# Kernel tuning notes

Hardware: AMD Instinct MI355X
Metric: run time of the kernel (lower is better)

## Reference

```python
import jax, jax.numpy as jnp
import numpy as np

B, S, D, P = 4, 2048, 1024, 1024

def setup_inputs() -> dict:
    key = jax.random.key(0)
    k1, k2, k3, k4 = jax.random.split(key, 4)
    x = jax.random.normal(k1, (B, S, D), dtype=jnp.float32)
    # nn.Linear weight is (out, in); store transposed (in, out) for x @ W
    scale = 1.0 / np.sqrt(D)
    Wq = jax.random.normal(k2, (D, P), dtype=jnp.float32) * scale
    Wk = jax.random.normal(k3, (D, P), dtype=jnp.float32) * scale
    Wv = jax.random.normal(k4, (D, P), dtype=jnp.float32) * scale
    return {"x": x, "Wq": Wq, "Wk": Wk, "Wv": Wv}

def reference(x, Wq, Wk, Wv):
    # projections (no bias)
    q = x @ Wq  # (B,S,P)
    k = x @ Wk
    v = x @ Wv
    scores = jnp.einsum('bsd,btd->bst', q, k)  # (B,S,S)
    seq = x.shape[1]
    causal = jnp.triu(jnp.ones((seq, seq), dtype=bool), k=1)
    scores = jnp.where(causal, -jnp.inf, scores)
    scores = scores / jnp.sqrt(jnp.asarray(P, dtype=scores.dtype))
    attn = jax.nn.softmax(scores, axis=-1)
    # dropout_prob=0.0 -> identity
    context = jnp.einsum('bst,btd->bsd', attn, v)  # (B,S,P)
    return context
```

## Files before the change

kernel.cpp:

```cpp
#include <hip/hip_runtime.h>
#include <hip/hip_bf16.h>


#define BDIM 4
#define SDIM 2048
#define DDIM 1024
#define PDIM 1024

typedef __attribute__((ext_vector_type(8))) short bf16x8;
typedef __attribute__((ext_vector_type(4))) float f32x4;
typedef __attribute__((ext_vector_type(16))) float f32x16;

__device__ __forceinline__ unsigned short f2bf(float f) {
    union { float f; unsigned int u; } v; v.f = f;
    unsigned int u = v.u;
    unsigned int r = (u + 0x7fffu + ((u >> 16) & 1u)) >> 16;
    return (unsigned short)r;
}

__device__ __forceinline__ float bf2f(unsigned short h) {
    union { unsigned int u; float f; } v;
    v.u = ((unsigned int)h) << 16;
    return v.f;
}

__device__ __forceinline__ void async16(const unsigned short* g, unsigned short* l) {
    __builtin_amdgcn_global_load_lds(
        (const __attribute__((address_space(1))) unsigned int*)g,
        (__attribute__((address_space(3))) unsigned int*)l,
        16, 0, 0);
}

__global__ __launch_bounds__(256) void prep_kernel(const float* __restrict__ x,
                                                   const float* __restrict__ W0,
                                                   const float* __restrict__ W1,
                                                   const float* __restrict__ W2,
                                                   unsigned short* __restrict__ Xb,
                                                   unsigned short* __restrict__ WT,
                                                   float* __restrict__ Lrow) {
    int bid = blockIdx.x;
    if (bid < 4096) {
        size_t i = (size_t)bid * 256 + threadIdx.x;
        float4 a = ((const float4*)x)[2 * i];
        float4 b = ((const float4*)x)[2 * i + 1];
        bf16x8 o;
        o[0] = (short)f2bf(a.x); o[1] = (short)f2bf(a.y);
        o[2] = (short)f2bf(a.z); o[3] = (short)f2bf(a.w);
        o[4] = (short)f2bf(b.x); o[5] = (short)f2bf(b.y);
        o[6] = (short)f2bf(b.z); o[7] = (short)f2bf(b.w);
        ((bf16x8*)Xb)[i] = o;
    } else if (bid < 4864) {
        int idx = bid - 4096;
        int wz = idx >> 8;
        int t  = idx & 255;
        const float* W = (wz == 0) ? W0 : (wz == 1) ? W1 : W2;
        unsigned short* Tz = WT + (size_t)wz * DDIM * PDIM;
        __shared__ float tle[64 * 65];
        int r0 = (t >> 4) * 64, c0 = (t & 15) * 64;
#pragma unroll
        for (int kk = 0; kk < 4; kk++) {
            int it = (int)threadIdx.x + 256 * kk;
            int r = it >> 4, c4 = (it & 15) * 4;
            float4 v = *(const float4*)(W + (size_t)(r0 + r) * PDIM + c0 + c4);
            float* dst = tle + r * 65 + c4;
            dst[0] = v.x; dst[1] = v.y; dst[2] = v.z; dst[3] = v.w;
        }
        __syncthreads();
#pragma unroll
        for (int kk = 0; kk < 2; kk++) {
            int it = (int)threadIdx.x + 256 * kk;
            int c = it >> 3, ch = (it & 7) * 8;
            bf16x8 o;
#pragma unroll
            for (int j = 0; j < 8; j++)
                o[j] = (short)f2bf(tle[(ch + j) * 65 + c]);
            *(bf16x8*)(Tz + (size_t)(c0 + c) * DDIM + r0 + ch) = o;
        }
    } else {
        float4 z4 = make_float4(0.f, 0.f, 0.f, 0.f);
#pragma unroll
        for (int kk = 0; kk < 8; kk++)
            ((float4*)Lrow)[(size_t)kk * 256 + threadIdx.x] = z4;
    }
}

template <int LDA, int LDB, int LDC, int KMAX, int MODE, typename CT>
__global__ __launch_bounds__(256) void gemm_bt(
    const unsigned short* __restrict__ A0, const unsigned short* __restrict__ A1,
    long long sA,
    const unsigned short* __restrict__ B0, long long sB,
    CT* __restrict__ C0, CT* __restrict__ C1, long long sC,
    unsigned short* __restrict__ Kb, unsigned short* __restrict__ VT,
    float* __restrict__ Lrow, float alpha) {
    const int BM = 128, BN = 128, BK = 64;
    const int ABUF = BM * BK;
    __shared__ __attribute__((aligned(16))) unsigned short smem[2 * ABUF + BN * BK];
    unsigned short* BsBuf = smem + 2 * ABUF;

    int tm, tn;
    if (MODE == 1) {
        int i = blockIdx.x;
        int t = (int)((sqrtf(8.f * i + 1.f) - 1.f) * 0.5f);
        if ((t + 1) * (t + 2) / 2 <= i) t++;
        if (t * (t + 1) / 2 > i) t--;
        tm = t * BM;
        tn = (i - t * (t + 1) / 2) * BN;
    } else if (MODE == 2) {
        int yy = (blockIdx.z < 2) ? ((int)gridDim.y - 1 - (int)blockIdx.y)
                                  : (int)blockIdx.y;
        tm = yy * BM;
        tn = blockIdx.x * BN;
    } else {
        tm = blockIdx.y * BM;
        tn = blockIdx.x * BN;
    }
    int kend = (MODE == 2) ? min(KMAX, tm + BM) : KMAX;

    int z = blockIdx.z;
    const unsigned short* A = (z < 2 ? A0 : A1) + (long long)(z & 1) * sA;
    const unsigned short* Bt = B0 + (long long)z * sB;
    CT* C = (z < 2 ? C0 : C1) + (long long)(z & 1) * sC;

    int tid  = threadIdx.x;
    int lane = tid & 63;
    int wave = tid >> 6;
    int wr   = (wave >> 1) * 64;
    int wc   = (wave & 1) * 64;
    int l31  = lane & 31;
    int hi   = lane >> 5;
    int rsw  = lane & 7;

    f32x16 acc[2][2] = {};

    int srow = tid >> 3;
    int scol = ((tid & 7) ^ (srow & 7)) * 8;
    const unsigned short* Ag = A + (size_t)(tm + srow) * LDA + scol;
    const unsigned short* Bg = Bt + (size_t)(tn + srow) * LDB + scol;

    auto issueA = [&](int k0, int buf) {
        unsigned short* la = smem + buf * ABUF + tid * 8;
        async16(Ag + k0, la);
        async16(Ag + k0 + 32 * LDA, la + 2048);
        async16(Ag + k0 + 64 * LDA, la + 4096);
        async16(Ag + k0 + 96 * LDA, la + 6144);
    };
    auto issueB = [&](int k0) {
        unsigned short* lb = BsBuf + tid * 8;
        async16(Bg + k0, lb);
        async16(Bg + k0 + 32 * LDB, lb + 2048);
        async16(Bg + k0 + 64 * LDB, lb + 4096);
        async16(Bg + k0 + 96 * LDB, lb + 6144);
    };

    auto kbody = [&](int i, int ns) {
        __syncthreads();
        bf16x8 bf[2][4];
#pragma unroll
        for (int nj = 0; nj < 2; nj++)
#pragma unroll
            for (int ks = 0; ks < 4; ks++)
                bf[nj][ks] = *(const bf16x8*)(BsBuf + (wc + nj * 32 + l31) * BK
                                                    + ((ks * 2 + hi) ^ rsw) * 8);
        __syncthreads();
        if (i + 1 < ns) { issueA((i + 1) * BK, (i + 1) & 1); issueB((i + 1) * BK); }
        const unsigned short* As = smem + (i & 1) * ABUF;
#pragma unroll
        for (int mi = 0; mi < 2; mi++) {
            bf16x8 af[4];
#pragma unroll
            for (int ks = 0; ks < 4; ks++)
                af[ks] = *(const bf16x8*)(As + (wr + mi * 32 + l31) * BK
                                             + ((ks * 2 + hi) ^ rsw) * 8);
#pragma unroll
            for (int ks = 0; ks < 4; ks++)
#pragma unroll
                for (int nj = 0; nj < 2; nj++)
                    acc[mi][nj] = __builtin_amdgcn_mfma_f32_32x32x16_bf16(
                        af[ks], bf[nj][ks], acc[mi][nj], 0, 0, 0);
        }
    };

    issueA(0, 0);
    issueB(0);
    if constexpr (MODE != 2) {
        constexpr int NS = KMAX / BK;
#pragma unroll
        for (int i = 0; i < NS; i++) kbody(i, NS);
    } else {
        int ns = kend / BK;
        for (int i = 0; i < ns; i++) kbody(i, ns);
    }

    if constexpr (MODE == 0) {
        if (tn < 2048) {
            unsigned short* D = (tn < 1024 ? (unsigned short*)C0 : Kb);
            int cbase = tn & 1023;
#pragma unroll
            for (int mi = 0; mi < 2; mi++) {
#pragma unroll
                for (int nj = 0; nj < 2; nj++) {
                    int c = cbase + wc + nj * 32 + l31;
#pragma unroll
                    for (int g = 0; g < 4; g++) {
                        int r0 = tm + wr + mi * 32 + g * 8 + hi * 4;
#pragma unroll
                        for (int rr = 0; rr < 4; rr++)
                            D[(size_t)(r0 + rr) * 1024 + c] =
                                f2bf(acc[mi][nj][g * 4 + rr]);
                    }
                }
            }
        } else {
            int b = tm >> 11;
            int s0 = tm & 2047;
            unsigned short* VTb = VT + (size_t)b * (PDIM * SDIM)
                                     + (size_t)(tn - 2048) * SDIM + s0;
            const int TP = 136;
            unsigned short* T = smem;
            __syncthreads();
#pragma unroll
            for (int p = 0; p < 4; p++) {
                if ((wave & 1) == (p >> 1)) {
                    int nj = p & 1;
#pragma unroll
                    for (int mi = 0; mi < 2; mi++) {
#pragma unroll
                        for (int g = 0; g < 4; g++) {
                            int rl = wr + mi * 32 + g * 8 + hi * 4;
                            ushort4 w;
                            w.x = f2bf(acc[mi][nj][g * 4 + 0]);
                            w.y = f2bf(acc[mi][nj][g * 4 + 1]);
                            w.z = f2bf(acc[mi][nj][g * 4 + 2]);
                            w.w = f2bf(acc[mi][nj][g * 4 + 3]);
                            *(ushort4*)(T + l31 * TP + rl) = w;
                        }
                    }
                }
                __syncthreads();
                {
                    int lr = tid >> 3;
                    int ck = (tid & 7) * 16;
                    bf16x8 u0 = *(const bf16x8*)(T + lr * TP + ck);
                    bf16x8 u1 = *(const bf16x8*)(T + lr * TP + ck + 8);
                    unsigned short* dst = VTb + (size_t)(32 * p + lr) * SDIM + ck;
                    *(bf16x8*)(dst) = u0;
                    *(bf16x8*)(dst + 8) = u1;
                }
                __syncthreads();
            }
        }
    } else if constexpr (MODE == 1) {
        float* Lb = Lrow + (size_t)z * SDIM;
        unsigned short* D = (unsigned short*)C;
#pragma unroll
        for (int mi = 0; mi < 2; mi++) {
#pragma unroll
            for (int g = 0; g < 4; g++) {
#pragma unroll
                for (int rr = 0; rr < 4; rr++) {
                    int r = tm + wr + mi * 32 + g * 8 + hi * 4 + rr;
                    float psum = 0.f;
#pragma unroll
                    for (int nj = 0; nj < 2; nj++) {
                        int c = tn + wc + nj * 32 + l31;
                        float p = 0.f;
                        if (c <= r)
                            p = __expf(acc[mi][nj][g * 4 + rr] * alpha - 8.0f);
                        psum += p;
                        D[(size_t)r * LDC + c] = f2bf(p);
                    }
#pragma unroll
                    for (int o = 16; o; o >>= 1) psum += __shfl_xor(psum, o, 64);
                    if (l31 == 0) atomicAdd(Lb + r, psum);
                }
            }
        }
    } else {
        const float* Lb = Lrow + (size_t)z * SDIM;
#pragma unroll
        for (int mi = 0; mi < 2; mi++) {
#pragma unroll
            for (int g = 0; g < 4; g++) {
#pragma unroll
                for (int rr = 0; rr < 4; rr++) {
                    int r = tm + wr + mi * 32 + g * 8 + hi * 4 + rr;
                    float inv = 1.0f / Lb[r];
#pragma unroll
                    for (int nj = 0; nj < 2; nj++) {
                        int c = tn + wc + nj * 32 + l31;
                        C[(size_t)r * LDC + c] = (CT)(acc[mi][nj][g * 4 + rr] * inv);
                    }
                }
            }
        }
    }
}

extern "C" void kernel_launch(void* const* d_in, const int* in_sizes, int n_in,
                              void* d_out, int out_size, void* d_ws, size_t ws_size,
                              hipStream_t stream) {
    const float* x  = (const float*)d_in[0];
    const float* Wq = (const float*)d_in[1];
    const float* Wk = (const float*)d_in[2];
    const float* Wv = (const float*)d_in[3];
    float* out = (float*)d_out;

    const size_t MS = (size_t)BDIM * SDIM;
    const long long SS = (long long)SDIM * SDIM;
    char* ws = (char*)d_ws;
    size_t off = 0;
    unsigned short* Xb   = (unsigned short*)(ws + off);
    unsigned short* S01  = Xb;                          off += MS * DDIM * 2;
    unsigned short* WT   = (unsigned short*)(ws + off); off += 3ull * DDIM * PDIM * 2;
    unsigned short* Q    = (unsigned short*)(ws + off); off += MS * PDIM * 2;
    unsigned short* Kb   = (unsigned short*)(ws + off); off += MS * PDIM * 2;
    unsigned short* VT   = (unsigned short*)(ws + off); off += MS * PDIM * 2;
    unsigned short* S23  = (unsigned short*)(ws + off); off += 2ull * SS * 2;
    float*          Lrow = (float*)(ws + off);          off += MS * sizeof(float);

    prep_kernel<<<4096 + 768 + 1, 256, 0, stream>>>(x, Wq, Wk, Wv, Xb, WT, Lrow);

    gemm_bt<DDIM, DDIM, PDIM, DDIM, 0, unsigned short>
        <<<dim3(3 * PDIM / 128, MS / 128, 1), 256, 0, stream>>>(
        Xb, Xb, 0, WT, 0, Q, Q, 0, Kb, VT, nullptr, 1.0f);

    const long long sQ = (long long)SDIM * PDIM;
    const float alpha = 1.0f / 32.0f;

    gemm_bt<PDIM, PDIM, SDIM, PDIM, 1, unsigned short>
        <<<dim3(136, 1, BDIM), 256, 0, stream>>>(
        Q, Q + 2 * sQ, sQ, Kb, sQ, S01, S23, SS, nullptr, nullptr, Lrow, alpha);

    const long long sOut = (long long)SDIM * PDIM;
    gemm_bt<SDIM, SDIM, PDIM, SDIM, 2, float>
        <<<dim3(PDIM / 128, SDIM / 128, BDIM), 256, 0, stream>>>(
        S01, S23, SS, VT, sQ, out, out + 2 * sOut, sOut, nullptr, nullptr, Lrow, 1.0f);
}
```

Before: 224.6 us.

## Fuse score and PV GEMMs into one kernel with per-row-tile flag sync

Merges the QK^T/exp kernel and the P·V kernel into a single launch. PV blocks spin on per-(batch,row-tile) atomic counters until every score tile in that row band is written, so PV work can start while other score tiles are still computing. This removes a kernel boundary and the tail idle time between the two stages. In exchange it relies on spin-waiting, which can deadlock or waste CUs if consumer blocks are scheduled before their producers. It also adds occupancy hints (launch_bounds 256,3) and refactors the GEMM core into a shared device function.

```diff
diff --git a/kernel.cpp b/kernel.cpp
--- a/kernel.cpp
+++ b/kernel.cpp
@@ -37,7 +37,8 @@
                                                    const float* __restrict__ W2,
                                                    unsigned short* __restrict__ Xb,
                                                    unsigned short* __restrict__ WT,
-                                                   float* __restrict__ Lrow) {
+                                                   float* __restrict__ Lrow,
+                                                   unsigned int* __restrict__ flags) {
     int bid = blockIdx.x;
     if (bid < 4096) {
         size_t i = (size_t)bid * 256 + threadIdx.x;
@@ -81,46 +82,19 @@
 #pragma unroll
         for (int kk = 0; kk < 8; kk++)
             ((float4*)Lrow)[(size_t)kk * 256 + threadIdx.x] = z4;
+        if (threadIdx.x < 64) flags[threadIdx.x] = 0;
     }
 }
 
-template <int LDA, int LDB, int LDC, int KMAX, int MODE, typename CT>
-__global__ __launch_bounds__(256) void gemm_bt(
-    const unsigned short* __restrict__ A0, const unsigned short* __restrict__ A1,
-    long long sA,
-    const unsigned short* __restrict__ B0, long long sB,
-    CT* __restrict__ C0, CT* __restrict__ C1, long long sC,
-    unsigned short* __restrict__ Kb, unsigned short* __restrict__ VT,
-    float* __restrict__ Lrow, float alpha) {
-    const int BM = 128, BN = 128, BK = 64;
-    const int ABUF = BM * BK;
-    __shared__ __attribute__((aligned(16))) unsigned short smem[2 * ABUF + BN * BK];
+template <int LDA, int LDB>
+__device__ __forceinline__ void run_core(
+    const unsigned short* __restrict__ A,
+    const unsigned short* __restrict__ Bt,
+    unsigned short* smem, int tm, int tn, int ns,
+    f32x16 (&acc)[2][2]) {
+    const int BK = 64;
+    const int ABUF = 128 * BK;
     unsigned short* BsBuf = smem + 2 * ABUF;
-
-    int tm, tn;
-    if (MODE == 1) {
-        int i = blockIdx.x;
-        int t = (int)((sqrtf(8.f * i + 1.f) - 1.f) * 0.5f);
-        if ((t + 1) * (t + 2) / 2 <= i) t++;
-        if (t * (t + 1) / 2 > i) t--;
-        tm = t * BM;
-        tn = (i - t * (t + 1) / 2) * BN;
-    } else if (MODE == 2) {
-        int yy = (blockIdx.z < 2) ? ((int)gridDim.y - 1 - (int)blockIdx.y)
-                                  : (int)blockIdx.y;
-        tm = yy * BM;
-        tn = blockIdx.x * BN;
-    } else {
-        tm = blockIdx.y * BM;
-        tn = blockIdx.x * BN;
-    }
-    int kend = (MODE == 2) ? min(KMAX, tm + BM) : KMAX;
-
-    int z = blockIdx.z;
-    const unsigned short* A = (z < 2 ? A0 : A1) + (long long)(z & 1) * sA;
-    const unsigned short* Bt = B0 + (long long)z * sB;
-    CT* C = (z < 2 ? C0 : C1) + (long long)(z & 1) * sC;
-
     int tid  = threadIdx.x;
     int lane = tid & 63;
     int wave = tid >> 6;
@@ -129,8 +103,6 @@
     int l31  = lane & 31;
     int hi   = lane >> 5;
     int rsw  = lane & 7;
-
-    f32x16 acc[2][2] = {};
 
     int srow = tid >> 3;
     int scol = ((tid & 7) ^ (srow & 7)) * 8;
@@ -152,7 +124,9 @@
         async16(Bg + k0 + 96 * LDB, lb + 6144);
     };
 
-    auto kbody = [&](int i, int ns) {
+    issueA(0, 0);
+    issueB(0);
+    for (int i = 0; i < ns; i++) {
         __syncthreads();
         bf16x8 bf[2][4];
 #pragma unroll
@@ -178,80 +152,120 @@
                     acc[mi][nj] = __builtin_amdgcn_mfma_f32_32x32x16_bf16(
                         af[ks], bf[nj][ks], acc[mi][nj], 0, 0, 0);
         }
-    };
-
-    issueA(0, 0);
-    issueB(0);
-    if constexpr (MODE != 2) {
-        constexpr int NS = KMAX / BK;
-#pragma unroll
-        for (int i = 0; i < NS; i++) kbody(i, NS);
+    }
+}
+
+__global__ __launch_bounds__(256) void qkv_kernel(
+    const unsigned short* __restrict__ Xb, const unsigned short* __restrict__ WT,
+    unsigned short* __restrict__ Q, unsigned short* __restrict__ Kb,
+    unsigned short* __restrict__ VT) {
+    const int ABUF = 128 * 64;
+    __shared__ __attribute__((aligned(16))) unsigned short smem[2 * ABUF + 128 * 64];
+    int tm = blockIdx.y * 128;
+    int tn = blockIdx.x * 128;
+    int tid  = threadIdx.x;
+    int lane = tid & 63;
+    int wave = tid >> 6;
+    int wr   = (wave >> 1) * 64;
+    int wc   = (wave & 1) * 64;
+    int l31  = lane & 31;
+    int hi   = lane >> 5;
+
+    f32x16 acc[2][2] = {};
+    run_core<DDIM, DDIM>(Xb, WT, smem, tm, tn, DDIM / 64, acc);
+
+    if (tn < 2048) {
+        unsigned short* D = (tn < 1024) ? Q : Kb;
+        int cbase = tn & 1023;
+#pragma unroll
+        for (int mi = 0; mi < 2; mi++) {
+#pragma unroll
+            for (int nj = 0; nj < 2; nj++) {
+                int c = cbase + wc + nj * 32 + l31;
+#pragma unroll
+                for (int g = 0; g < 4; g++) {
+                    int r0 = tm + wr + mi * 32 + g * 8 + hi * 4;
+#pragma unroll
+                    for (int rr = 0; rr < 4; rr++)
+                        D[(size_t)(r0 + rr) * 1024 + c] = f2bf(acc[mi][nj][g * 4 + rr]);
+                }
+            }
+        }
     } else {
-        int ns = kend / BK;
-        for (int i = 0; i < ns; i++) kbody(i, ns);
-    }
-
-    if constexpr (MODE == 0) {
-        if (tn < 2048) {
-            unsigned short* D = (tn < 1024 ? (unsigned short*)C0 : Kb);
-            int cbase = tn & 1023;
-#pragma unroll
-            for (int mi = 0; mi < 2; mi++) {
-#pragma unroll
-                for (int nj = 0; nj < 2; nj++) {
-                    int c = cbase + wc + nj * 32 + l31;
+        int b = tm >> 11;
+        int s0 = tm & 2047;
+        unsigned short* VTb = VT + (size_t)b * (PDIM * SDIM)
+                                 + (size_t)(tn - 2048) * SDIM + s0;
+        const int TP = 136;
+        unsigned short* T = smem;
+        __syncthreads();
+#pragma unroll
+        for (int p = 0; p < 4; p++) {
+            if ((wave & 1) == (p >> 1)) {
+                int nj = p & 1;
+#pragma unroll
+                for (int mi = 0; mi < 2; mi++) {
 #pragma unroll
                     for (int g = 0; g < 4; g++) {
-                        int r0 = tm + wr + mi * 32 + g * 8 + hi * 4;
-#pragma unroll
-                        for (int rr = 0; rr < 4; rr++)
-                            D[(size_t)(r0 + rr) * 1024 + c] =
-                                f2bf(acc[mi][nj][g * 4 + rr]);
+                        int rl = wr + mi * 32 + g * 8 + hi * 4;
+                        ushort4 w;
+                        w.x = f2bf(acc[mi][nj][g * 4 + 0]);
+                        w.y = f2bf(acc[mi][nj][g * 4 + 1]);
+                        w.z = f2bf(acc[mi][nj][g * 4 + 2]);
+                        w.w = f2bf(acc[mi][nj][g * 4 + 3]);
+                        *(ushort4*)(T + l31 * TP + rl) = w;
                     }
                 }
             }
-        } else {
-            int b = tm >> 11;
-            int s0 = tm & 2047;
-            unsigned short* VTb = VT + (size_t)b * (PDIM * SDIM)
-                                     + (size_t)(tn - 2048) * SDIM + s0;
-            const int TP = 136;
-            unsigned short* T = smem;
             __syncthreads();
-#pragma unroll
-            for (int p = 0; p < 4; p++) {
-                if ((wave & 1) == (p >> 1)) {
-                    int nj = p & 1;
-#pragma unroll
-                    for (int mi = 0; mi < 2; mi++) {
-#pragma unroll
-                        for (int g = 0; g < 4; g++) {
-                            int rl = wr + mi * 32 + g * 8 + hi * 4;
-                            ushort4 w;
-                            w.x = f2bf(acc[mi][nj][g * 4 + 0]);
-                            w.y = f2bf(acc[mi][nj][g * 4 + 1]);
-                            w.z = f2bf(acc[mi][nj][g * 4 + 2]);
-                            w.w = f2bf(acc[mi][nj][g * 4 + 3]);
-                            *(ushort4*)(T + l31 * TP + rl) = w;
-                        }
-                    }
-                }
-                __syncthreads();
-                {
-                    int lr = tid >> 3;
-                    int ck = (tid & 7) * 16;
-                    bf16x8 u0 = *(const bf16x8*)(T + lr * TP + ck);
-                    bf16x8 u1 = *(const bf16x8*)(T + lr * TP + ck + 8);
-                    unsigned short* dst = VTb + (size_t)(32 * p + lr) * SDIM + ck;
-                    *(bf16x8*)(dst) = u0;
-                    *(bf16x8*)(dst + 8) = u1;
-                }
-                __syncthreads();
-            }
-        }
-    } else if constexpr (MODE == 1) {
+            {
+                int lr = tid >> 3;
+                int ck = (tid & 7) * 16;
+                bf16x8 u0 = *(const bf16x8*)(T + lr * TP + ck);
+                bf16x8 u1 = *(const bf16x8*)(T + lr * TP + ck + 8);
+                unsigned short* dst = VTb + (size_t)(32 * p + lr) * SDIM + ck;
+                *(bf16x8*)(dst) = u0;
+                *(bf16x8*)(dst + 8) = u1;
+            }
+            __syncthreads();
+        }
+    }
+}
+
+__global__ __launch_bounds__(256, 3) void tail_kernel(
+    const unsigned short* __restrict__ Q, const unsigned short* __restrict__ Kb,
+    unsigned short* __restrict__ P01, unsigned short* __restrict__ P23,
+    const unsigned short* __restrict__ VT, float* __restrict__ out,
+    float* __restrict__ Lrow, unsigned int* __restrict__ flags, float alpha) {
+    const int ABUF = 128 * 64;
+    __shared__ __attribute__((aligned(16))) unsigned short smem[2 * ABUF + 128 * 64];
+    const long long sQ = (long long)SDIM * PDIM;
+    const long long SS = (long long)SDIM * SDIM;
+    int z = blockIdx.z;
+    int tid  = threadIdx.x;
+    int lane = tid & 63;
+    int wave = tid >> 6;
+    int wr   = (wave >> 1) * 64;
+    int wc   = (wave & 1) * 64;
+    int l31  = lane & 31;
+    int hi   = lane >> 5;
+
+    if (blockIdx.x < 136) {
+        int i = blockIdx.x;
+        int t = (int)((sqrtf(8.f * i + 1.f) - 1.f) * 0.5f);
+        if ((t + 1) * (t + 2) / 2 <= i) t++;
+        if (t * (t + 1) / 2 > i) t--;
+        int tm = t * 128;
+        int tn = (i - t * (t + 1) / 2) * 128;
+
+        const unsigned short* A  = Q + (long long)z * sQ;
+        const unsigned short* Bt = Kb + (long long)z * sQ;
+        unsigned short* P = (z < 2 ? P01 : P23) + (long long)(z & 1) * SS;
+
+        f32x16 acc[2][2] = {};
+        run_core<PDIM, PDIM>(A, Bt, smem, tm, tn, PDIM / 64, acc);
+
         float* Lb = Lrow + (size_t)z * SDIM;
-        unsigned short* D = (unsigned short*)C;
 #pragma unroll
         for (int mi = 0; mi < 2; mi++) {
 #pragma unroll
@@ -267,7 +281,7 @@
                         if (c <= r)
                             p = __expf(acc[mi][nj][g * 4 + rr] * alpha - 8.0f);
                         psum += p;
-                        D[(size_t)r * LDC + c] = f2bf(p);
+                        P[(size_t)r * SDIM + c] = f2bf(p);
                     }
 #pragma unroll
                     for (int o = 16; o; o >>= 1) psum += __shfl_xor(psum, o, 64);
@@ -275,7 +289,31 @@
                 }
             }
         }
+        __syncthreads();
+        if (tid == 0) {
+            __threadfence();
+            atomicAdd(&flags[z * 16 + t], 1u);
+        }
     } else {
+        int idx = blockIdx.x - 136;
+        int yy = idx >> 3, xx = idx & 7;
+        int tm = yy * 128, tn = xx * 128;
+
+        if (tid == 0) {
+            while (__hip_atomic_load(&flags[z * 16 + yy], __ATOMIC_ACQUIRE,
+                                     __HIP_MEMORY_SCOPE_AGENT) < (unsigned)(yy + 1))
+                __builtin_amdgcn_s_sleep(4);
+        }
+        __syncthreads();
+        __threadfence();
+
+        const unsigned short* A  = (z < 2 ? P01 : P23) + (long long)(z & 1) * SS;
+        const unsigned short* Bt = VT + (long long)z * sQ;
+        float* O = out + (long long)z * sQ;
+
+        f32x16 acc[2][2] = {};
+        run_core<SDIM, SDIM>(A, Bt, smem, tm, tn, (tm + 128) / 64, acc);
+
         const float* Lb = Lrow + (size_t)z * SDIM;
 #pragma unroll
         for (int mi = 0; mi < 2; mi++) {
@@ -288,7 +326,7 @@
 #pragma unroll
                     for (int nj = 0; nj < 2; nj++) {
                         int c = tn + wc + nj * 32 + l31;
-                        C[(size_t)r * LDC + c] = (CT)(acc[mi][nj][g * 4 + rr] * inv);
+                        O[(size_t)r * PDIM + c] = acc[mi][nj][g * 4 + rr] * inv;
                     }
                 }
             }
@@ -317,22 +355,15 @@
     unsigned short* VT   = (unsigned short*)(ws + off); off += MS * PDIM * 2;
     unsigned short* S23  = (unsigned short*)(ws + off); off += 2ull * SS * 2;
     float*          Lrow = (float*)(ws + off);          off += MS * sizeof(float);
-
-    prep_kernel<<<4096 + 768 + 1, 256, 0, stream>>>(x, Wq, Wk, Wv, Xb, WT, Lrow);
-
-    gemm_bt<DDIM, DDIM, PDIM, DDIM, 0, unsigned short>
-        <<<dim3(3 * PDIM / 128, MS / 128, 1), 256, 0, stream>>>(
-        Xb, Xb, 0, WT, 0, Q, Q, 0, Kb, VT, nullptr, 1.0f);
-
-    const long long sQ = (long long)SDIM * PDIM;
+    unsigned int*   flags = (unsigned int*)(ws + off);  off += 64 * sizeof(unsigned);
+
+    prep_kernel<<<4096 + 768 + 1, 256, 0, stream>>>(x, Wq, Wk, Wv, Xb, WT, Lrow, flags);
+
+    qkv_kernel<<<dim3(3 * PDIM / 128, MS / 128, 1), 256, 0, stream>>>(
+        Xb, WT, Q, Kb, VT);
+
     const float alpha = 1.0f / 32.0f;
 
-    gemm_bt<PDIM, PDIM, SDIM, PDIM, 1, unsigned short>
-        <<<dim3(136, 1, BDIM), 256, 0, stream>>>(
-        Q, Q + 2 * sQ, sQ, Kb, sQ, S01, S23, SS, nullptr, nullptr, Lrow, alpha);
-
-    const long long sOut = (long long)SDIM * PDIM;
-    gemm_bt<SDIM, SDIM, PDIM, SDIM, 2, float>
-        <<<dim3(PDIM / 128, SDIM / 128, BDIM), 256, 0, stream>>>(
-        S01, S23, SS, VT, sQ, out, out + 2 * sOut, sOut, nullptr, nullptr, Lrow, 1.0f);
-}
+    tail_kernel<<<dim3(136 + 128, 1, BDIM), 256, 0, stream>>>(
+        Q, Kb, S01, S23, VT, out, Lrow, flags, alpha);
+}
```

Result: slower. 483.4 us (+115.2%).
